# Performance work log

Measured on AMD Instinct MI355X. Metric: run time of the kernel, lower is better.

The kernel has to match this reference:

```python
import jax, jax.numpy as jnp
import numpy as np

B, T, D = 32, 2048, 512
BATCH_SIZE = 32  # config.batch_size: number of MVN draws


def setup_inputs() -> dict:
    key = jax.random.key(0)
    k1, k2 = jax.random.split(key)
    x = jax.random.normal(k1, (B, T, D), dtype=jnp.float32)
    z = jax.random.normal(k2, (BATCH_SIZE, D), dtype=jnp.float32)  # standard-normal noise for reparameterized MVN draw
    return {"x": x, "z": z}


def reference(x, z):
    # mean over batch and time -> [D]
    mean = jnp.mean(x, axis=(0, 1))
    # per-batch covariance over time axis, then mean over batch -> [D, D]
    t = x.shape[1]
    xc = x - jnp.mean(x, axis=1, keepdims=True)
    # sum over b and t fused: equals mean_b( xc_b^T xc_b / (t-1) )
    cov = jnp.einsum('btd,bte->de', xc, xc) / ((t - 1) * x.shape[0])
    # multivariate normal draw via Cholesky reparameterization:
    # sample = mean + z @ L^T, L L^T = cov
    L = jnp.linalg.cholesky(cov)
    return mean + z @ L.T
```

## Files before the change

### kernel.cpp

```cpp
#include <hip/hip_runtime.h>

#define Dn 512
#define Bn 32
#define Tn 2048
#define BT 65536
#define NCHUNK 64
#define CHUNK_K 1024

typedef unsigned short u16;
typedef __attribute__((ext_vector_type(8))) short short8;
typedef __attribute__((ext_vector_type(4))) float floatx4;

__device__ __forceinline__ u16 f2bf(float f) {
    unsigned u = __float_as_uint(f);
    unsigned r = (u + 0x7FFFu + ((u >> 16) & 1u)) >> 16;
    return (u16)r;
}
__device__ __forceinline__ float bf2f(u16 s) { return __uint_as_float(((unsigned)s) << 16); }

#define GLL(gp, sp) __builtin_amdgcn_global_load_lds( \
    (const __attribute__((address_space(1))) void*)(gp), \
    (__attribute__((address_space(3))) void*)(sp), 16, 0, 0)

#define REP64(X) X(0) X(1) X(2) X(3) X(4) X(5) X(6) X(7) X(8) X(9) X(10) X(11) X(12) X(13) X(14) X(15) \
    X(16) X(17) X(18) X(19) X(20) X(21) X(22) X(23) X(24) X(25) X(26) X(27) X(28) X(29) X(30) X(31) \
    X(32) X(33) X(34) X(35) X(36) X(37) X(38) X(39) X(40) X(41) X(42) X(43) X(44) X(45) X(46) X(47) \
    X(48) X(49) X(50) X(51) X(52) X(53) X(54) X(55) X(56) X(57) X(58) X(59) X(60) X(61) X(62) X(63)
#define REPJ(OP, K) OP(K,0) OP(K,1) OP(K,2) OP(K,3) OP(K,4) OP(K,5) OP(K,6) OP(K,7) OP(K,8) OP(K,9) \
    OP(K,10) OP(K,11) OP(K,12) OP(K,13) OP(K,14) OP(K,15) OP(K,16) OP(K,17) OP(K,18) OP(K,19) \
    OP(K,20) OP(K,21) OP(K,22) OP(K,23) OP(K,24) OP(K,25) OP(K,26) OP(K,27) OP(K,28) OP(K,29) \
    OP(K,30) OP(K,31) OP(K,32) OP(K,33) OP(K,34) OP(K,35) OP(K,36) OP(K,37) OP(K,38) OP(K,39) \
    OP(K,40) OP(K,41) OP(K,42) OP(K,43) OP(K,44) OP(K,45) OP(K,46) OP(K,47) OP(K,48) OP(K,49) \
    OP(K,50) OP(K,51) OP(K,52) OP(K,53) OP(K,54) OP(K,55) OP(K,56) OP(K,57) OP(K,58) OP(K,59) \
    OP(K,60) OP(K,61) OP(K,62) OP(K,63)
#define REPQ(OP, C) OP(C,0,0,0) OP(C,1,0,1) OP(C,2,0,2) OP(C,3,0,3) OP(C,4,1,0) OP(C,5,1,1) OP(C,6,1,2) OP(C,7,1,3) \
    OP(C,8,2,0) OP(C,9,2,1) OP(C,10,2,2) OP(C,11,2,3) OP(C,12,3,0) OP(C,13,3,1) OP(C,14,3,2) OP(C,15,3,3) \
    OP(C,16,4,0) OP(C,17,4,1) OP(C,18,4,2) OP(C,19,4,3) OP(C,20,5,0) OP(C,21,5,1) OP(C,22,5,2) OP(C,23,5,3) \
    OP(C,24,6,0) OP(C,25,6,1) OP(C,26,6,2) OP(C,27,6,3) OP(C,28,7,0) OP(C,29,7,1) OP(C,30,7,2) OP(C,31,7,3) \
    OP(C,32,8,0) OP(C,33,8,1) OP(C,34,8,2) OP(C,35,8,3) OP(C,36,9,0) OP(C,37,9,1) OP(C,38,9,2) OP(C,39,9,3) \
    OP(C,40,10,0) OP(C,41,10,1) OP(C,42,10,2) OP(C,43,10,3) OP(C,44,11,0) OP(C,45,11,1) OP(C,46,11,2) OP(C,47,11,3) \
    OP(C,48,12,0) OP(C,49,12,1) OP(C,50,12,2) OP(C,51,12,3) OP(C,52,13,0) OP(C,53,13,1) OP(C,54,13,2) OP(C,55,13,3) \
    OP(C,56,14,0) OP(C,57,14,1) OP(C,58,14,2) OP(C,59,14,3) OP(C,60,15,0) OP(C,61,15,1) OP(C,62,15,2) OP(C,63,15,3)
#define REPW(OP) OP(0,0,1,2,3) OP(1,4,5,6,7) OP(2,8,9,10,11) OP(3,12,13,14,15) OP(4,16,17,18,19) \
    OP(5,20,21,22,23) OP(6,24,25,26,27) OP(7,28,29,30,31) OP(8,32,33,34,35) OP(9,36,37,38,39) \
    OP(10,40,41,42,43) OP(11,44,45,46,47) OP(12,48,49,50,51) OP(13,52,53,54,55) OP(14,56,57,58,59) \
    OP(15,60,61,62,63)
#define REP16C(OP, C) OP(C,0) OP(C,1) OP(C,2) OP(C,3) OP(C,4) OP(C,5) OP(C,6) OP(C,7) \
    OP(C,8) OP(C,9) OP(C,10) OP(C,11) OP(C,12) OP(C,13) OP(C,14) OP(C,15)

__global__ __launch_bounds__(256) void k_zero(float* __restrict__ mu) {
    floatx4 z = {0.f, 0.f, 0.f, 0.f};
    ((floatx4*)mu)[blockIdx.x * 256 + threadIdx.x] = z;
}

__global__ __launch_bounds__(256) void k_transpose(const float* __restrict__ x,
                                                   u16* __restrict__ Xt,
                                                   float* __restrict__ mu) {
    int tt = blockIdx.x;
    int dt = blockIdx.y;
    int b  = blockIdx.z;
    __shared__ u16 sT[64][68];
    int tid = threadIdx.x;
    int row = tid >> 4;
    int c4  = (tid & 15) * 4;
    const float* src = x + ((long)b * Tn + (long)tt * 64) * Dn + dt * 64;
#pragma unroll
    for (int q = 0; q < 4; q++) {
        int r = row + q * 16;
        floatx4 v = *(const floatx4*)(src + (long)r * Dn + c4);
        sT[c4 + 0][r] = f2bf(v[0]);
        sT[c4 + 1][r] = f2bf(v[1]);
        sT[c4 + 2][r] = f2bf(v[2]);
        sT[c4 + 3][r] = f2bf(v[3]);
    }
    __syncthreads();
    int drow = tid >> 3;
    int koff = (tid & 7) * 8;
    long kout = (long)b * Tn + (long)tt * 64 + koff;
#pragma unroll
    for (int p = 0; p < 2; p++) {
        int dr = drow + p * 32;
        u16 tmp[8];
        float s = 0.f;
#pragma unroll
        for (int j = 0; j < 8; j++) {
            tmp[j] = sT[dr][koff + j];
            s += bf2f(tmp[j]);
        }
        *(short8*)(Xt + (long)(dt * 64 + dr) * BT + kout) = *(short8*)tmp;
        s += __shfl_down(s, 4, 64);
        s += __shfl_down(s, 2, 64);
        s += __shfl_down(s, 1, 64);
        if ((tid & 7) == 0) atomicAdd(mu + b * 512 + dt * 64 + dr, s);
    }
}

__global__ __launch_bounds__(256, 3) void k_gram(const u16* __restrict__ Xt,
                                                 float* __restrict__ partial) {
    int chunk = blockIdx.x;
    int pos = blockIdx.y;
    int di = (pos < 4) ? 0 : (pos < 7) ? 1 : (pos < 9) ? 2 : 3;
    int start = di * 4 - (di * (di - 1)) / 2;
    int ei = di + (pos - start);
    int d0 = di * 128, e0 = ei * 128;

    __shared__ u16 sA[128 * 32];
    __shared__ u16 sB[128 * 32];
    int tid = threadIdx.x;
    int w = tid >> 6, l = tid & 63;
    int wm = w & 1, wn = w >> 1;
    long kbase = (long)chunk * CHUNK_K;
    int srow = w * 16 + (l >> 2);
    int sk = (l & 3) * 8;
    const u16* gA0 = Xt + (long)(d0 + srow) * BT + kbase + sk;
    const u16* gA1 = gA0 + 64l * BT;
    const u16* gB0 = Xt + (long)(e0 + srow) * BT + kbase + sk;
    const u16* gB1 = gB0 + 64l * BT;
    u16* sA0 = sA + (w * 16) * 32;
    u16* sA1 = sA0 + 64 * 32;
    u16* sB0 = sB + (w * 16) * 32;
    u16* sB1 = sB0 + 64 * 32;
    int m = l & 15, g = l >> 4;
    const u16* fA = sA + (wm * 64 + m) * 32 + g * 8;
    const u16* fB = sB + (wn * 64 + m) * 32 + g * 8;

    floatx4 acc[4][4] = {};
    for (int kk = 0; kk < CHUNK_K; kk += 32) {
        GLL(gA0 + kk, sA0);
        GLL(gA1 + kk, sA1);
        GLL(gB0 + kk, sB0);
        GLL(gB1 + kk, sB1);
        __syncthreads();
        short8 af[4], bfv[4];
#pragma unroll
        for (int i = 0; i < 4; i++) af[i] = *(const short8*)(fA + i * 16 * 32);
#pragma unroll
        for (int j = 0; j < 4; j++) bfv[j] = *(const short8*)(fB + j * 16 * 32);
#pragma unroll
        for (int i = 0; i < 4; i++)
#pragma unroll
            for (int j = 0; j < 4; j++)
                acc[i][j] = __builtin_amdgcn_mfma_f32_16x16x32_bf16(af[i], bfv[j], acc[i][j], 0, 0, 0);
        __syncthreads();
    }
    float* P = partial + (long)chunk * (512l * 512);
    int col = l & 15, rowg = (l >> 4) * 4;
#pragma unroll
    for (int i = 0; i < 4; i++)
#pragma unroll
        for (int j = 0; j < 4; j++) {
            int rr = d0 + wm * 64 + i * 16 + rowg;
            int cc = e0 + wn * 64 + j * 16 + col;
#pragma unroll
            for (int r = 0; r < 4; r++) P[(long)(rr + r) * 512 + cc] = acc[i][j][r];
        }
}

__global__ __launch_bounds__(256) void k_assemble(const float* __restrict__ partial,
                                                  const float* __restrict__ mu,
                                                  float* __restrict__ A) {
    int d = blockIdx.y;
    int e = blockIdx.x * 256 + threadIdx.x;
    int bd = d >> 7, be = e >> 7;
    long idx = (bd <= be) ? ((long)d * 512 + e) : ((long)e * 512 + d);
    float s = 0.f;
#pragma unroll
    for (int c = 0; c < NCHUNK; c++) s += partial[c * (512l * 512) + idx];
    float msum = 0.f;
#pragma unroll
    for (int b = 0; b < 32; b++) msum += mu[b * 512 + d] * mu[b * 512 + e];
    A[(long)d * 512 + e] = (s - msum * (1.0f / Tn)) * (1.0f / ((Tn - 1.0f) * Bn));
}

__global__ __launch_bounds__(64, 1) void k_chol_panel(float* __restrict__ A, int kb) {
    const int k0 = kb * 64;
    const int lane = threadIdx.x;
    __shared__ float sD[64 * 68];
    __shared__ float sInv[64];
    const floatx4 z4 = {0.f, 0.f, 0.f, 0.f};

    const float* Dr = A + (long)(k0 + lane) * 512 + k0;
#define LDV(Q,A0,A1,A2,A3) floatx4 v##Q = *(const floatx4*)(Dr + 4*(Q));
    REPW(LDV)
#undef LDV
#define DECR(C,M,Mq,e) float r##M = v##Mq[(e)];
    REPQ(DECR, 0)
#undef DECR

    float vinv = 0.f;
#define SH1(K,J) float t##J = ((J) > (K)) ? __shfl(lik, (J), 64) : 0.0f;
#define FM1(K,J) if ((J) > (K)) r##J = fmaf(-lik, t##J, r##J);
#define STEP(K) { float akk = __shfl(r##K, (K), 64); float sd = sqrtf(akk); \
                  float inv = 1.0f / sd; float lik = (lane == (K)) ? sd : r##K * inv; \
                  r##K = lik; if (lane == (K)) vinv = inv; REPJ(SH1, K) REPJ(FM1, K) }
    REP64(STEP)
#undef STEP
#undef FM1
#undef SH1

    if (blockIdx.x == 0) {
        float* W = A + (long)(k0 + lane) * 512 + k0;
#define STW(Q,A0,A1,A2,A3) { floatx4 w; w[0]=r##A0; w[1]=r##A1; w[2]=r##A2; w[3]=r##A3; \
                             *(floatx4*)(W + 4*(Q)) = w; }
        REPW(STW)
#undef STW
        return;
    }

#define STD(Q,A0,A1,A2,A3) { floatx4 w; w[0]=r##A0; w[1]=r##A1; w[2]=r##A2; w[3]=r##A3; \
                             *(floatx4*)(sD + lane * 68 + 4*(Q)) = w; }
    REPW(STD)
#undef STD
    sInv[lane] = vinv;
    __syncthreads();

    int rbase = k0 + 64 + (blockIdx.x - 1) * 64;
    const float* R = A + (long)(rbase + lane) * 512 + k0;
#define LDA(Q,A0,A1,A2,A3) floatx4 u##Q = *(const floatx4*)(R + 4*(Q));
    REPW(LDA)
#undef LDA
#define DECA(C,M,Mq,e) float a##M = u##Mq[(e)];
    REPQ(DECA, 0)
#undef DECA
#define LQ(C,Q) floatx4 q##Q = ((C) > 4*(Q)) ? *(const floatx4*)(sD + (C) * 68 + 4*(Q)) : z4;
#define TF(C,M,Mq,e) if ((M) < (C)) acc##e = fmaf(a##M, q##Mq[(e)], acc##e);
#define TSTEP(C) { REP16C(LQ, C) float acc0 = 0.f, acc1 = 0.f, acc2 = 0.f, acc3 = 0.f; \
                   REPQ(TF, C) a##C = (a##C - ((acc0 + acc1) + (acc2 + acc3))) * sInv[(C)]; }
    REP64(TSTEP)
#undef TSTEP
#undef TF
#undef LQ

    float* Wr = A + (long)(rbase + lane) * 512 + k0;
#define STA(Q,A0,A1,A2,A3) { floatx4 w; w[0]=a##A0; w[1]=a##A1; w[2]=a##A2; w[3]=a##A3; \
                             *(floatx4*)(Wr + 4*(Q)) = w; }
    REPW(STA)
#undef STA
}

__global__ __launch_bounds__(256) void k_chol_update(float* __restrict__ A, int kb) {
    int k0 = kb * 64, base = k0 + 64;
    int idx = blockIdx.x, ti = 0;
    while (idx > ti) { idx -= ti + 1; ti++; }
    int tj = idx;
    int r0 = base + ti * 64, c0 = base + tj * 64;
    __shared__ float sI[64][65];
    __shared__ float sJ[64][65];
    int tid = threadIdx.x;
    int row = tid >> 4, c4 = (tid & 15) * 4;
#pragma unroll
    for (int q = 0; q < 4; q++) {
        int rr = row + q * 16;
        *(floatx4*)&sI[rr][c4] = *(const floatx4*)(A + (long)(r0 + rr) * 512 + k0 + c4);
        *(floatx4*)&sJ[rr][c4] = *(const floatx4*)(A + (long)(c0 + rr) * 512 + k0 + c4);
    }
    __syncthreads();
    int ri = (tid >> 4) * 4, cj = (tid & 15) * 4;
    float acc[4][4] = {};
    for (int k = 0; k < 64; k += 4) {
        floatx4 av[4], bv[4];
#pragma unroll
        for (int ii = 0; ii < 4; ii++) av[ii] = *(const floatx4*)&sI[ri + ii][k];
#pragma unroll
        for (int jj = 0; jj < 4; jj++) bv[jj] = *(const floatx4*)&sJ[cj + jj][k];
#pragma unroll
        for (int ii = 0; ii < 4; ii++)
#pragma unroll
            for (int jj = 0; jj < 4; jj++)
#pragma unroll
                for (int q = 0; q < 4; q++)
                    acc[ii][jj] = fmaf(av[ii][q], bv[jj][q], acc[ii][jj]);
    }
#pragma unroll
    for (int ii = 0; ii < 4; ii++) {
        float* dst = A + (long)(r0 + ri + ii) * 512 + c0 + cj;
        floatx4 old = *(const floatx4*)dst;
#pragma unroll
        for (int jj = 0; jj < 4; jj++) old[jj] -= acc[ii][jj];
        *(floatx4*)dst = old;
    }
}

__global__ __launch_bounds__(512) void k_output(const float* __restrict__ z,
                                                const float* __restrict__ A,
                                                const float* __restrict__ mu,
                                                float* __restrict__ out) {
    int i = blockIdx.x, d = threadIdx.x;
    __shared__ float sz[512];
    sz[d] = z[(long)i * 512 + d];
    __syncthreads();
    float mean = 0.f;
#pragma unroll
    for (int b = 0; b < 32; b++) mean += mu[b * 512 + d];
    mean *= (1.0f / (32.0f * 2048.0f));
    const float* Lr = A + (long)d * 512;
    float acc = 0.f;
    int dmax = d + 1;
    int e4 = dmax & ~3;
    for (int e = 0; e < e4; e += 4) {
        floatx4 l = *(const floatx4*)(Lr + e);
        acc += l[0] * sz[e] + l[1] * sz[e + 1] + l[2] * sz[e + 2] + l[3] * sz[e + 3];
    }
    for (int e = e4; e < dmax; e++) acc += Lr[e] * sz[e];
    out[(long)i * 512 + d] = mean + acc;
}

extern "C" void kernel_launch(void* const* d_in, const int* in_sizes, int n_in,
                              void* d_out, int out_size, void* d_ws, size_t ws_size,
                              hipStream_t stream) {
    const float* x = (const float*)d_in[0];
    const float* z = (const float*)d_in[1];
    float* out = (float*)d_out;
    char* ws = (char*)d_ws;
    u16* Xt = (u16*)ws;
    float* mu = (float*)(ws + 67108864);
    float* partial = (float*)(ws + 67108864 + 65536);
    float* A = (float*)(ws + 67108864 + 65536 + 67108864);

    k_zero<<<16, 256, 0, stream>>>(mu);
    k_transpose<<<dim3(32, 8, 32), 256, 0, stream>>>(x, Xt, mu);
    k_gram<<<dim3(NCHUNK, 10), 256, 0, stream>>>(Xt, partial);
    k_assemble<<<dim3(2, 512), 256, 0, stream>>>(partial, mu, A);
    for (int kb = 0; kb < 8; kb++) {
        int nb = 7 - kb;
        k_chol_panel<<<nb + 1, 64, 0, stream>>>(A, kb);
        int tiles = nb * (nb + 1) / 2;
        if (tiles > 0) k_chol_update<<<tiles, 256, 0, stream>>>(A, kb);
    }
    k_output<<<32, 512, 0, stream>>>(z, A, mu, out);
}
```

Measured before the change: 665.0 us.

## Fuse assemble, blocked Cholesky and output into one persistent kernel with grid barriers

Replaces the assemble kernel, the per-step panel/update launches (about 16 launches) and the output kernel with a single 64-block persistent kernel. Phases are separated by an atomic-counter grid barrier in global memory. This removes kernel launch gaps on the serial Cholesky chain. In exchange, the grid barriers add spin-wait latency, and correctness relies on all 64 blocks being co-resident. Panel work is now split across 2 blocks with 4 wavefronts each.

```diff
diff --git a/kernel.cpp b/kernel.cpp
--- a/kernel.cpp
+++ b/kernel.cpp
@@ -6,6 +6,7 @@
 #define BT 65536
 #define NCHUNK 64
 #define CHUNK_K 1024
+#define NBLK 64
 
 typedef unsigned short u16;
 typedef __attribute__((ext_vector_type(8))) short short8;
@@ -21,6 +22,18 @@
 #define GLL(gp, sp) __builtin_amdgcn_global_load_lds( \
     (const __attribute__((address_space(1))) void*)(gp), \
     (__attribute__((address_space(3))) void*)(sp), 16, 0, 0)
+
+__device__ __forceinline__ void gbar(int* bar, int target) {
+    __syncthreads();
+    if (threadIdx.x == 0) {
+        __threadfence();
+        __hip_atomic_fetch_add(bar, 1, __ATOMIC_ACQ_REL, __HIP_MEMORY_SCOPE_AGENT);
+        while (__hip_atomic_load(bar, __ATOMIC_ACQUIRE, __HIP_MEMORY_SCOPE_AGENT) < target)
+            __builtin_amdgcn_s_sleep(2);
+        __threadfence();
+    }
+    __syncthreads();
+}
 
 #define REP64(X) X(0) X(1) X(2) X(3) X(4) X(5) X(6) X(7) X(8) X(9) X(10) X(11) X(12) X(13) X(14) X(15) \
     X(16) X(17) X(18) X(19) X(20) X(21) X(22) X(23) X(24) X(25) X(26) X(27) X(28) X(29) X(30) X(31) \
@@ -48,9 +61,10 @@
 #define REP16C(OP, C) OP(C,0) OP(C,1) OP(C,2) OP(C,3) OP(C,4) OP(C,5) OP(C,6) OP(C,7) \
     OP(C,8) OP(C,9) OP(C,10) OP(C,11) OP(C,12) OP(C,13) OP(C,14) OP(C,15)
 
-__global__ __launch_bounds__(256) void k_zero(float* __restrict__ mu) {
+__global__ __launch_bounds__(256) void k_zero(float* __restrict__ mu, int* __restrict__ bar) {
     floatx4 z = {0.f, 0.f, 0.f, 0.f};
     ((floatx4*)mu)[blockIdx.x * 256 + threadIdx.x] = z;
+    if (blockIdx.x == 0 && threadIdx.x == 0) *bar = 0;
 }
 
 __global__ __launch_bounds__(256) void k_transpose(const float* __restrict__ x,
@@ -156,153 +170,169 @@
         }
 }
 
-__global__ __launch_bounds__(256) void k_assemble(const float* __restrict__ partial,
-                                                  const float* __restrict__ mu,
-                                                  float* __restrict__ A) {
-    int d = blockIdx.y;
-    int e = blockIdx.x * 256 + threadIdx.x;
-    int bd = d >> 7, be = e >> 7;
-    long idx = (bd <= be) ? ((long)d * 512 + e) : ((long)e * 512 + d);
-    float s = 0.f;
-#pragma unroll
-    for (int c = 0; c < NCHUNK; c++) s += partial[c * (512l * 512) + idx];
-    float msum = 0.f;
-#pragma unroll
-    for (int b = 0; b < 32; b++) msum += mu[b * 512 + d] * mu[b * 512 + e];
-    A[(long)d * 512 + e] = (s - msum * (1.0f / Tn)) * (1.0f / ((Tn - 1.0f) * Bn));
-}
-
-__global__ __launch_bounds__(64, 1) void k_chol_panel(float* __restrict__ A, int kb) {
-    const int k0 = kb * 64;
-    const int lane = threadIdx.x;
-    __shared__ float sD[64 * 68];
-    __shared__ float sInv[64];
+__global__ __launch_bounds__(256, 1) void k_backend(const float* __restrict__ partial,
+                                                    const float* __restrict__ mu,
+                                                    const float* __restrict__ z,
+                                                    float* __restrict__ A,
+                                                    float* __restrict__ out,
+                                                    int* __restrict__ bar) {
+    __shared__ float smem[8320];
+    const int tid = threadIdx.x;
+    const int blk = blockIdx.x;
+    int ph = 0;
     const floatx4 z4 = {0.f, 0.f, 0.f, 0.f};
 
-    const float* Dr = A + (long)(k0 + lane) * 512 + k0;
+#pragma unroll 2
+    for (int i = 0; i < 16; i++) {
+        int f = blk * 4096 + i * 256 + tid;
+        int d = f >> 9, e = f & 511;
+        int bd = d >> 7, be = e >> 7;
+        long idx = (bd <= be) ? ((long)d * 512 + e) : ((long)e * 512 + d);
+        float s = 0.f;
+#pragma unroll
+        for (int c = 0; c < NCHUNK; c++) s += partial[c * (512l * 512) + idx];
+        float msum = 0.f;
+#pragma unroll
+        for (int b = 0; b < 32; b++) msum += mu[b * 512 + d] * mu[b * 512 + e];
+        A[(long)d * 512 + e] = (s - msum * (1.0f / Tn)) * (1.0f / ((Tn - 1.0f) * Bn));
+    }
+    gbar(bar, (++ph) * NBLK);
+
+    for (int kb = 0; kb < 8; kb++) {
+        const int k0 = kb * 64;
+        const int nb = 7 - kb;
+        if (blk < 2) {
+            const int lane = tid & 63;
+            const int unit = blk * 4 + (tid >> 6);
+            float* sD = smem;
+            float* sInv = smem + 64 * 68;
+
+            const float* Dr = A + (long)(k0 + lane) * 512 + k0;
 #define LDV(Q,A0,A1,A2,A3) floatx4 v##Q = *(const floatx4*)(Dr + 4*(Q));
-    REPW(LDV)
+            REPW(LDV)
 #undef LDV
 #define DECR(C,M,Mq,e) float r##M = v##Mq[(e)];
-    REPQ(DECR, 0)
+            REPQ(DECR, 0)
 #undef DECR
-
-    float vinv = 0.f;
+            float vinv = 0.f;
 #define SH1(K,J) float t##J = ((J) > (K)) ? __shfl(lik, (J), 64) : 0.0f;
 #define FM1(K,J) if ((J) > (K)) r##J = fmaf(-lik, t##J, r##J);
 #define STEP(K) { float akk = __shfl(r##K, (K), 64); float sd = sqrtf(akk); \
                   float inv = 1.0f / sd; float lik = (lane == (K)) ? sd : r##K * inv; \
                   r##K = lik; if (lane == (K)) vinv = inv; REPJ(SH1, K) REPJ(FM1, K) }
-    REP64(STEP)
+            REP64(STEP)
 #undef STEP
 #undef FM1
 #undef SH1
 
-    if (blockIdx.x == 0) {
-        float* W = A + (long)(k0 + lane) * 512 + k0;
+            if (unit == 0) {
+                float* W = A + (long)(k0 + lane) * 512 + k0;
 #define STW(Q,A0,A1,A2,A3) { floatx4 w; w[0]=r##A0; w[1]=r##A1; w[2]=r##A2; w[3]=r##A3; \
                              *(floatx4*)(W + 4*(Q)) = w; }
-        REPW(STW)
+                REPW(STW)
 #undef STW
-        return;
-    }
-
+            }
 #define STD(Q,A0,A1,A2,A3) { floatx4 w; w[0]=r##A0; w[1]=r##A1; w[2]=r##A2; w[3]=r##A3; \
                              *(floatx4*)(sD + lane * 68 + 4*(Q)) = w; }
-    REPW(STD)
+            REPW(STD)
 #undef STD
-    sInv[lane] = vinv;
-    __syncthreads();
-
-    int rbase = k0 + 64 + (blockIdx.x - 1) * 64;
-    const float* R = A + (long)(rbase + lane) * 512 + k0;
+            sInv[lane] = vinv;
+            __syncthreads();
+
+            if (unit >= 1 && unit <= nb) {
+                int rbase = k0 + 64 + (unit - 1) * 64;
+                const float* R = A + (long)(rbase + lane) * 512 + k0;
 #define LDA(Q,A0,A1,A2,A3) floatx4 u##Q = *(const floatx4*)(R + 4*(Q));
-    REPW(LDA)
+                REPW(LDA)
 #undef LDA
 #define DECA(C,M,Mq,e) float a##M = u##Mq[(e)];
-    REPQ(DECA, 0)
+                REPQ(DECA, 0)
 #undef DECA
 #define LQ(C,Q) floatx4 q##Q = ((C) > 4*(Q)) ? *(const floatx4*)(sD + (C) * 68 + 4*(Q)) : z4;
 #define TF(C,M,Mq,e) if ((M) < (C)) acc##e = fmaf(a##M, q##Mq[(e)], acc##e);
 #define TSTEP(C) { REP16C(LQ, C) float acc0 = 0.f, acc1 = 0.f, acc2 = 0.f, acc3 = 0.f; \
                    REPQ(TF, C) a##C = (a##C - ((acc0 + acc1) + (acc2 + acc3))) * sInv[(C)]; }
-    REP64(TSTEP)
+                REP64(TSTEP)
 #undef TSTEP
 #undef TF
 #undef LQ
-
-    float* Wr = A + (long)(rbase + lane) * 512 + k0;
+                float* Wr = A + (long)(rbase + lane) * 512 + k0;
 #define STA(Q,A0,A1,A2,A3) { floatx4 w; w[0]=a##A0; w[1]=a##A1; w[2]=a##A2; w[3]=a##A3; \
                              *(floatx4*)(Wr + 4*(Q)) = w; }
-    REPW(STA)
+                REPW(STA)
 #undef STA
-}
-
-__global__ __launch_bounds__(256) void k_chol_update(float* __restrict__ A, int kb) {
-    int k0 = kb * 64, base = k0 + 64;
-    int idx = blockIdx.x, ti = 0;
-    while (idx > ti) { idx -= ti + 1; ti++; }
-    int tj = idx;
-    int r0 = base + ti * 64, c0 = base + tj * 64;
-    __shared__ float sI[64][65];
-    __shared__ float sJ[64][65];
-    int tid = threadIdx.x;
-    int row = tid >> 4, c4 = (tid & 15) * 4;
-#pragma unroll
-    for (int q = 0; q < 4; q++) {
-        int rr = row + q * 16;
-        *(floatx4*)&sI[rr][c4] = *(const floatx4*)(A + (long)(r0 + rr) * 512 + k0 + c4);
-        *(floatx4*)&sJ[rr][c4] = *(const floatx4*)(A + (long)(c0 + rr) * 512 + k0 + c4);
-    }
-    __syncthreads();
-    int ri = (tid >> 4) * 4, cj = (tid & 15) * 4;
-    float acc[4][4] = {};
-    for (int k = 0; k < 64; k += 4) {
-        floatx4 av[4], bv[4];
-#pragma unroll
-        for (int ii = 0; ii < 4; ii++) av[ii] = *(const floatx4*)&sI[ri + ii][k];
-#pragma unroll
-        for (int jj = 0; jj < 4; jj++) bv[jj] = *(const floatx4*)&sJ[cj + jj][k];
-#pragma unroll
-        for (int ii = 0; ii < 4; ii++)
-#pragma unroll
-            for (int jj = 0; jj < 4; jj++)
-#pragma unroll
-                for (int q = 0; q < 4; q++)
-                    acc[ii][jj] = fmaf(av[ii][q], bv[jj][q], acc[ii][jj]);
-    }
-#pragma unroll
-    for (int ii = 0; ii < 4; ii++) {
-        float* dst = A + (long)(r0 + ri + ii) * 512 + c0 + cj;
-        floatx4 old = *(const floatx4*)dst;
-#pragma unroll
-        for (int jj = 0; jj < 4; jj++) old[jj] -= acc[ii][jj];
-        *(floatx4*)dst = old;
-    }
-}
-
-__global__ __launch_bounds__(512) void k_output(const float* __restrict__ z,
-                                                const float* __restrict__ A,
-                                                const float* __restrict__ mu,
-                                                float* __restrict__ out) {
-    int i = blockIdx.x, d = threadIdx.x;
-    __shared__ float sz[512];
-    sz[d] = z[(long)i * 512 + d];
-    __syncthreads();
-    float mean = 0.f;
-#pragma unroll
-    for (int b = 0; b < 32; b++) mean += mu[b * 512 + d];
-    mean *= (1.0f / (32.0f * 2048.0f));
-    const float* Lr = A + (long)d * 512;
-    float acc = 0.f;
-    int dmax = d + 1;
-    int e4 = dmax & ~3;
-    for (int e = 0; e < e4; e += 4) {
-        floatx4 l = *(const floatx4*)(Lr + e);
-        acc += l[0] * sz[e] + l[1] * sz[e + 1] + l[2] * sz[e + 2] + l[3] * sz[e + 3];
-    }
-    for (int e = e4; e < dmax; e++) acc += Lr[e] * sz[e];
-    out[(long)i * 512 + d] = mean + acc;
+            }
+        }
+        gbar(bar, (++ph) * NBLK);
+
+        const int tiles = nb * (nb + 1) / 2;
+        if (tiles > 0) {
+            if (blk < tiles) {
+                int idx = blk, ti = 0;
+                while (idx > ti) { idx -= ti + 1; ti++; }
+                int tj = idx;
+                int r0 = k0 + 64 + ti * 64, c0 = k0 + 64 + tj * 64;
+                float* sI = smem;
+                float* sJ = smem + 4160;
+                int row = tid >> 4, c4 = (tid & 15) * 4;
+#pragma unroll
+                for (int q = 0; q < 4; q++) {
+                    int rr = row + q * 16;
+                    *(floatx4*)&sI[rr * 65 + c4] = *(const floatx4*)(A + (long)(r0 + rr) * 512 + k0 + c4);
+                    *(floatx4*)&sJ[rr * 65 + c4] = *(const floatx4*)(A + (long)(c0 + rr) * 512 + k0 + c4);
+                }
+                __syncthreads();
+                int ri = (tid >> 4) * 4, cj = (tid & 15) * 4;
+                float acc[4][4] = {};
+                for (int k = 0; k < 64; k += 4) {
+                    floatx4 av[4], bv[4];
+#pragma unroll
+                    for (int ii = 0; ii < 4; ii++) av[ii] = *(const floatx4*)&sI[(ri + ii) * 65 + k];
+#pragma unroll
+                    for (int jj = 0; jj < 4; jj++) bv[jj] = *(const floatx4*)&sJ[(cj + jj) * 65 + k];
+#pragma unroll
+                    for (int ii = 0; ii < 4; ii++)
+#pragma unroll
+                        for (int jj = 0; jj < 4; jj++)
+#pragma unroll
+                            for (int q = 0; q < 4; q++)
+                                acc[ii][jj] = fmaf(av[ii][q], bv[jj][q], acc[ii][jj]);
+                }
+#pragma unroll
+                for (int ii = 0; ii < 4; ii++) {
+                    float* dst = A + (long)(r0 + ri + ii) * 512 + c0 + cj;
+                    floatx4 old = *(const floatx4*)dst;
+#pragma unroll
+                    for (int jj = 0; jj < 4; jj++) old[jj] -= acc[ii][jj];
+                    *(floatx4*)dst = old;
+                }
+            }
+            gbar(bar, (++ph) * NBLK);
+        }
+    }
+
+    {
+        int i = blk >> 1, half = blk & 1;
+        float* sz = smem;
+        sz[tid] = z[(long)i * 512 + tid];
+        sz[tid + 256] = z[(long)i * 512 + tid + 256];
+        __syncthreads();
+        int d = half * 256 + tid;
+        float mean = 0.f;
+#pragma unroll
+        for (int b = 0; b < 32; b++) mean += mu[b * 512 + d];
+        mean *= (1.0f / (32.0f * 2048.0f));
+        const float* Lr = A + (long)d * 512;
+        float acc = 0.f;
+        int dmax = d + 1;
+        int e4 = dmax & ~3;
+        for (int e = 0; e < e4; e += 4) {
+            floatx4 lv = *(const floatx4*)(Lr + e);
+            acc += lv[0] * sz[e] + lv[1] * sz[e + 1] + lv[2] * sz[e + 2] + lv[3] * sz[e + 3];
+        }
+        for (int e = e4; e < dmax; e++) acc += Lr[e] * sz[e];
+        out[(long)i * 512 + d] = mean + acc;
+    }
 }
 
 extern "C" void kernel_launch(void* const* d_in, const int* in_sizes, int n_in,
@@ -316,16 +346,10 @@
     float* mu = (float*)(ws + 67108864);
     float* partial = (float*)(ws + 67108864 + 65536);
     float* A = (float*)(ws + 67108864 + 65536 + 67108864);
-
-    k_zero<<<16, 256, 0, stream>>>(mu);
+    int* bar = (int*)(ws + 67108864 + 65536 + 67108864 + 1048576);
+
+    k_zero<<<16, 256, 0, stream>>>(mu, bar);
     k_transpose<<<dim3(32, 8, 32), 256, 0, stream>>>(x, Xt, mu);
     k_gram<<<dim3(NCHUNK, 10), 256, 0, stream>>>(Xt, partial);
-    k_assemble<<<dim3(2, 512), 256, 0, stream>>>(partial, mu, A);
-    for (int kb = 0; kb < 8; kb++) {
-        int nb = 7 - kb;
-        k_chol_panel<<<nb + 1, 64, 0, stream>>>(A, kb);
-        int tiles = nb * (nb + 1) / 2;
-        if (tiles > 0) k_chol_update<<<tiles, 256, 0, stream>>>(A, kb);
-    }
-    k_output<<<32, 512, 0, stream>>>(z, A, mu, out);
-}
+    k_backend<<<NBLK, 256, 0, stream>>>(partial, mu, z, A, out, bar);
+}
```

Measured after the change: 1.184 ms. 78.1% more time.

## Fuse blocked Cholesky panel and update launches into one persistent single-block kernel

Applied to the files above, without the earlier changes.

Replaces the per-step panel and trailing-update kernel launches (about 15 in total) with one 512-thread single-block kernel. It loops over the 8 block columns and separates stages with __syncthreads. The triangular solve now pulls diagonal-block values from the same wave by lane shuffles instead of staging them through shared memory. The aim is to remove launch and inter-kernel gaps. The cost is that all trailing-update tiles now run on one CU, two at a time, instead of spread over many blocks, and register pressure under the 512-thread launch bound may cause spills.

```diff
diff --git a/kernel.cpp b/kernel.cpp
--- a/kernel.cpp
+++ b/kernel.cpp
@@ -33,20 +33,19 @@
     OP(K,40) OP(K,41) OP(K,42) OP(K,43) OP(K,44) OP(K,45) OP(K,46) OP(K,47) OP(K,48) OP(K,49) \
     OP(K,50) OP(K,51) OP(K,52) OP(K,53) OP(K,54) OP(K,55) OP(K,56) OP(K,57) OP(K,58) OP(K,59) \
     OP(K,60) OP(K,61) OP(K,62) OP(K,63)
-#define REPQ(OP, C) OP(C,0,0,0) OP(C,1,0,1) OP(C,2,0,2) OP(C,3,0,3) OP(C,4,1,0) OP(C,5,1,1) OP(C,6,1,2) OP(C,7,1,3) \
-    OP(C,8,2,0) OP(C,9,2,1) OP(C,10,2,2) OP(C,11,2,3) OP(C,12,3,0) OP(C,13,3,1) OP(C,14,3,2) OP(C,15,3,3) \
-    OP(C,16,4,0) OP(C,17,4,1) OP(C,18,4,2) OP(C,19,4,3) OP(C,20,5,0) OP(C,21,5,1) OP(C,22,5,2) OP(C,23,5,3) \
-    OP(C,24,6,0) OP(C,25,6,1) OP(C,26,6,2) OP(C,27,6,3) OP(C,28,7,0) OP(C,29,7,1) OP(C,30,7,2) OP(C,31,7,3) \
-    OP(C,32,8,0) OP(C,33,8,1) OP(C,34,8,2) OP(C,35,8,3) OP(C,36,9,0) OP(C,37,9,1) OP(C,38,9,2) OP(C,39,9,3) \
-    OP(C,40,10,0) OP(C,41,10,1) OP(C,42,10,2) OP(C,43,10,3) OP(C,44,11,0) OP(C,45,11,1) OP(C,46,11,2) OP(C,47,11,3) \
-    OP(C,48,12,0) OP(C,49,12,1) OP(C,50,12,2) OP(C,51,12,3) OP(C,52,13,0) OP(C,53,13,1) OP(C,54,13,2) OP(C,55,13,3) \
+#define REPQA(OP, C) OP(C,0,0,0) OP(C,1,0,1) OP(C,2,0,2) OP(C,3,0,3) OP(C,4,1,0) OP(C,5,1,1) OP(C,6,1,2) OP(C,7,1,3) \
+    OP(C,8,2,0) OP(C,9,2,1) OP(C,10,2,2) OP(C,11,2,3) OP(C,12,3,0) OP(C,13,3,1) OP(C,14,3,2) OP(C,15,3,3)
+#define REPQB(OP, C) OP(C,16,4,0) OP(C,17,4,1) OP(C,18,4,2) OP(C,19,4,3) OP(C,20,5,0) OP(C,21,5,1) OP(C,22,5,2) OP(C,23,5,3) \
+    OP(C,24,6,0) OP(C,25,6,1) OP(C,26,6,2) OP(C,27,6,3) OP(C,28,7,0) OP(C,29,7,1) OP(C,30,7,2) OP(C,31,7,3)
+#define REPQC(OP, C) OP(C,32,8,0) OP(C,33,8,1) OP(C,34,8,2) OP(C,35,8,3) OP(C,36,9,0) OP(C,37,9,1) OP(C,38,9,2) OP(C,39,9,3) \
+    OP(C,40,10,0) OP(C,41,10,1) OP(C,42,10,2) OP(C,43,10,3) OP(C,44,11,0) OP(C,45,11,1) OP(C,46,11,2) OP(C,47,11,3)
+#define REPQD(OP, C) OP(C,48,12,0) OP(C,49,12,1) OP(C,50,12,2) OP(C,51,12,3) OP(C,52,13,0) OP(C,53,13,1) OP(C,54,13,2) OP(C,55,13,3) \
     OP(C,56,14,0) OP(C,57,14,1) OP(C,58,14,2) OP(C,59,14,3) OP(C,60,15,0) OP(C,61,15,1) OP(C,62,15,2) OP(C,63,15,3)
+#define REPQ(OP, C) REPQA(OP, C) REPQB(OP, C) REPQC(OP, C) REPQD(OP, C)
 #define REPW(OP) OP(0,0,1,2,3) OP(1,4,5,6,7) OP(2,8,9,10,11) OP(3,12,13,14,15) OP(4,16,17,18,19) \
     OP(5,20,21,22,23) OP(6,24,25,26,27) OP(7,28,29,30,31) OP(8,32,33,34,35) OP(9,36,37,38,39) \
     OP(10,40,41,42,43) OP(11,44,45,46,47) OP(12,48,49,50,51) OP(13,52,53,54,55) OP(14,56,57,58,59) \
     OP(15,60,61,62,63)
-#define REP16C(OP, C) OP(C,0) OP(C,1) OP(C,2) OP(C,3) OP(C,4) OP(C,5) OP(C,6) OP(C,7) \
-    OP(C,8) OP(C,9) OP(C,10) OP(C,11) OP(C,12) OP(C,13) OP(C,14) OP(C,15)
 
 __global__ __launch_bounds__(256) void k_zero(float* __restrict__ mu) {
     floatx4 z = {0.f, 0.f, 0.f, 0.f};
@@ -172,112 +171,125 @@
     A[(long)d * 512 + e] = (s - msum * (1.0f / Tn)) * (1.0f / ((Tn - 1.0f) * Bn));
 }
 
-__global__ __launch_bounds__(64, 1) void k_chol_panel(float* __restrict__ A, int kb) {
-    const int k0 = kb * 64;
-    const int lane = threadIdx.x;
-    __shared__ float sD[64 * 68];
-    __shared__ float sInv[64];
-    const floatx4 z4 = {0.f, 0.f, 0.f, 0.f};
-
-    const float* Dr = A + (long)(k0 + lane) * 512 + k0;
+__global__ __launch_bounds__(512, 2) void k_chol(float* __restrict__ A) {
+    __shared__ float sU[16640];
+    const int tid = threadIdx.x;
+    const int lane = tid & 63;
+    const int wave = tid >> 6;
+    const int grp = tid >> 8;
+    const int gtid = tid & 255;
+
+    for (int kb = 0; kb < 8; kb++) {
+        const int k0 = kb * 64;
+        const int nb = 7 - kb;
+
+        if (wave <= nb) {
+            const float* Dr = A + (long)(k0 + lane) * 512 + k0;
 #define LDV(Q,A0,A1,A2,A3) floatx4 v##Q = *(const floatx4*)(Dr + 4*(Q));
-    REPW(LDV)
+            REPW(LDV)
 #undef LDV
 #define DECR(C,M,Mq,e) float r##M = v##Mq[(e)];
-    REPQ(DECR, 0)
+            REPQ(DECR, 0)
 #undef DECR
-
-    float vinv = 0.f;
+            float vinv = 0.f;
 #define SH1(K,J) float t##J = ((J) > (K)) ? __shfl(lik, (J), 64) : 0.0f;
 #define FM1(K,J) if ((J) > (K)) r##J = fmaf(-lik, t##J, r##J);
 #define STEP(K) { float akk = __shfl(r##K, (K), 64); float sd = sqrtf(akk); \
                   float inv = 1.0f / sd; float lik = (lane == (K)) ? sd : r##K * inv; \
                   r##K = lik; if (lane == (K)) vinv = inv; REPJ(SH1, K) REPJ(FM1, K) }
-    REP64(STEP)
+            REP64(STEP)
 #undef STEP
 #undef FM1
 #undef SH1
 
-    if (blockIdx.x == 0) {
-        float* W = A + (long)(k0 + lane) * 512 + k0;
+            if (wave == 0) {
+                float* W = A + (long)(k0 + lane) * 512 + k0;
 #define STW(Q,A0,A1,A2,A3) { floatx4 w; w[0]=r##A0; w[1]=r##A1; w[2]=r##A2; w[3]=r##A3; \
                              *(floatx4*)(W + 4*(Q)) = w; }
-        REPW(STW)
+                REPW(STW)
 #undef STW
-        return;
-    }
-
-#define STD(Q,A0,A1,A2,A3) { floatx4 w; w[0]=r##A0; w[1]=r##A1; w[2]=r##A2; w[3]=r##A3; \
-                             *(floatx4*)(sD + lane * 68 + 4*(Q)) = w; }
-    REPW(STD)
-#undef STD
-    sInv[lane] = vinv;
-    __syncthreads();
-
-    int rbase = k0 + 64 + (blockIdx.x - 1) * 64;
-    const float* R = A + (long)(rbase + lane) * 512 + k0;
+            }
+
+            if (wave >= 1) {
+                const int rbase = k0 + 64 + (wave - 1) * 64;
+                const float* R = A + (long)(rbase + lane) * 512 + k0;
 #define LDA(Q,A0,A1,A2,A3) floatx4 u##Q = *(const floatx4*)(R + 4*(Q));
-    REPW(LDA)
+                REPW(LDA)
 #undef LDA
 #define DECA(C,M,Mq,e) float a##M = u##Mq[(e)];
-    REPQ(DECA, 0)
+                REPQ(DECA, 0)
 #undef DECA
-#define LQ(C,Q) floatx4 q##Q = ((C) > 4*(Q)) ? *(const floatx4*)(sD + (C) * 68 + 4*(Q)) : z4;
-#define TF(C,M,Mq,e) if ((M) < (C)) acc##e = fmaf(a##M, q##Mq[(e)], acc##e);
-#define TSTEP(C) { REP16C(LQ, C) float acc0 = 0.f, acc1 = 0.f, acc2 = 0.f, acc3 = 0.f; \
-                   REPQ(TF, C) a##C = (a##C - ((acc0 + acc1) + (acc2 + acc3))) * sInv[(C)]; }
-    REP64(TSTEP)
-#undef TSTEP
-#undef TF
-#undef LQ
-
-    float* Wr = A + (long)(rbase + lane) * 512 + k0;
+#define TSH(C,M,Mq,e) float t##M = ((M) < (C)) ? __shfl(r##M, (C), 64) : 0.0f;
+#define TFM(C,M,Mq,e) if ((M) < (C)) acc##e = fmaf(a##M, t##M, acc##e);
+#define TST(C) { float acc0 = 0.f, acc1 = 0.f, acc2 = 0.f, acc3 = 0.f; \
+    { REPQA(TSH, C) REPQA(TFM, C) } { REPQB(TSH, C) REPQB(TFM, C) } \
+    { REPQC(TSH, C) REPQC(TFM, C) } { REPQD(TSH, C) REPQD(TFM, C) } \
+    float invC = __shfl(vinv, (C), 64); \
+    a##C = (a##C - ((acc0 + acc1) + (acc2 + acc3))) * invC; }
+                REP64(TST)
+#undef TST
+#undef TFM
+#undef TSH
+                float* Wr = A + (long)(rbase + lane) * 512 + k0;
 #define STA(Q,A0,A1,A2,A3) { floatx4 w; w[0]=a##A0; w[1]=a##A1; w[2]=a##A2; w[3]=a##A3; \
                              *(floatx4*)(Wr + 4*(Q)) = w; }
-    REPW(STA)
+                REPW(STA)
 #undef STA
-}
-
-__global__ __launch_bounds__(256) void k_chol_update(float* __restrict__ A, int kb) {
-    int k0 = kb * 64, base = k0 + 64;
-    int idx = blockIdx.x, ti = 0;
-    while (idx > ti) { idx -= ti + 1; ti++; }
-    int tj = idx;
-    int r0 = base + ti * 64, c0 = base + tj * 64;
-    __shared__ float sI[64][65];
-    __shared__ float sJ[64][65];
-    int tid = threadIdx.x;
-    int row = tid >> 4, c4 = (tid & 15) * 4;
-#pragma unroll
-    for (int q = 0; q < 4; q++) {
-        int rr = row + q * 16;
-        *(floatx4*)&sI[rr][c4] = *(const floatx4*)(A + (long)(r0 + rr) * 512 + k0 + c4);
-        *(floatx4*)&sJ[rr][c4] = *(const floatx4*)(A + (long)(c0 + rr) * 512 + k0 + c4);
-    }
-    __syncthreads();
-    int ri = (tid >> 4) * 4, cj = (tid & 15) * 4;
-    float acc[4][4] = {};
-    for (int k = 0; k < 64; k += 4) {
-        floatx4 av[4], bv[4];
-#pragma unroll
-        for (int ii = 0; ii < 4; ii++) av[ii] = *(const floatx4*)&sI[ri + ii][k];
-#pragma unroll
-        for (int jj = 0; jj < 4; jj++) bv[jj] = *(const floatx4*)&sJ[cj + jj][k];
-#pragma unroll
-        for (int ii = 0; ii < 4; ii++)
-#pragma unroll
-            for (int jj = 0; jj < 4; jj++)
-#pragma unroll
-                for (int q = 0; q < 4; q++)
-                    acc[ii][jj] = fmaf(av[ii][q], bv[jj][q], acc[ii][jj]);
-    }
-#pragma unroll
-    for (int ii = 0; ii < 4; ii++) {
-        float* dst = A + (long)(r0 + ri + ii) * 512 + c0 + cj;
-        floatx4 old = *(const floatx4*)dst;
-#pragma unroll
-        for (int jj = 0; jj < 4; jj++) old[jj] -= acc[ii][jj];
-        *(floatx4*)dst = old;
+            }
+        }
+        __syncthreads();
+
+        const int tiles = nb * (nb + 1) / 2;
+        const int rounds = (tiles + 1) >> 1;
+        for (int rd = 0; rd < rounds; rd++) {
+            int t = rd * 2 + grp;
+            int ti = 0, tj = 0;
+            if (t < tiles) {
+                int idx = t;
+                while (idx > ti) { idx -= ti + 1; ti++; }
+                tj = idx;
+            }
+            int r0 = k0 + 64 + ti * 64, c0 = k0 + 64 + tj * 64;
+            float* sI = &sU[grp * 8320];
+            float* sJ = &sU[grp * 8320 + 4160];
+            if (t < tiles) {
+                int row = gtid >> 4, c4 = (gtid & 15) * 4;
+#pragma unroll
+                for (int q = 0; q < 4; q++) {
+                    int rr = row + q * 16;
+                    *(floatx4*)&sI[rr * 65 + c4] = *(const floatx4*)(A + (long)(r0 + rr) * 512 + k0 + c4);
+                    *(floatx4*)&sJ[rr * 65 + c4] = *(const floatx4*)(A + (long)(c0 + rr) * 512 + k0 + c4);
+                }
+            }
+            __syncthreads();
+            if (t < tiles) {
+                int ri = (gtid >> 4) * 4, cj = (gtid & 15) * 4;
+                float acc[4][4] = {};
+                for (int k = 0; k < 64; k += 4) {
+                    floatx4 av[4], bv[4];
+#pragma unroll
+                    for (int ii = 0; ii < 4; ii++) av[ii] = *(const floatx4*)&sI[(ri + ii) * 65 + k];
+#pragma unroll
+                    for (int jj = 0; jj < 4; jj++) bv[jj] = *(const floatx4*)&sJ[(cj + jj) * 65 + k];
+#pragma unroll
+                    for (int ii = 0; ii < 4; ii++)
+#pragma unroll
+                        for (int jj = 0; jj < 4; jj++)
+#pragma unroll
+                            for (int q = 0; q < 4; q++)
+                                acc[ii][jj] = fmaf(av[ii][q], bv[jj][q], acc[ii][jj]);
+                }
+#pragma unroll
+                for (int ii = 0; ii < 4; ii++) {
+                    float* dst = A + (long)(r0 + ri + ii) * 512 + c0 + cj;
+                    floatx4 old = *(const floatx4*)dst;
+#pragma unroll
+                    for (int jj = 0; jj < 4; jj++) old[jj] -= acc[ii][jj];
+                    *(floatx4*)dst = old;
+                }
+            }
+            __syncthreads();
+        }
     }
 }
 
@@ -321,11 +333,6 @@
     k_transpose<<<dim3(32, 8, 32), 256, 0, stream>>>(x, Xt, mu);
     k_gram<<<dim3(NCHUNK, 10), 256, 0, stream>>>(Xt, partial);
     k_assemble<<<dim3(2, 512), 256, 0, stream>>>(partial, mu, A);
-    for (int kb = 0; kb < 8; kb++) {
-        int nb = 7 - kb;
-        k_chol_panel<<<nb + 1, 64, 0, stream>>>(A, kb);
-        int tiles = nb * (nb + 1) / 2;
-        if (tiles > 0) k_chol_update<<<tiles, 256, 0, stream>>>(A, kb);
-    }
+    k_chol<<<1, 512, 0, stream>>>(A);
     k_output<<<32, 512, 0, stream>>>(z, A, mu, out);
 }
```

Measured after the change: 1.799 ms. +170.5%, slower.
